# Kernel tuning notes

Hardware: AMD Instinct MI355X
Metric: run time of the kernel (lower is better)

The kernel has to match this reference:

```python
import jax, jax.numpy as jnp
import numpy as np

B, L, P, D, RD, NT = 128, 128, 1024, 128, 128, 256
SCALE = 1.0 / float(np.sqrt(D))


def _gelu(x):
    return jax.nn.gelu(x, approximate=False)


def _ln(x, g, b):
    mu = jnp.mean(x, axis=-1, keepdims=True)
    v = jnp.mean((x - mu) ** 2, axis=-1, keepdims=True)
    return (x - mu) * jax.lax.rsqrt(v + 1e-5) * g + b


def _mlp2(x, w1, b1, w2, b2):
    return _gelu(x @ w1 + b1) @ w2 + b2


def _l2norm(x):
    return x / jnp.maximum(jnp.sqrt(jnp.sum(x * x, axis=-1, keepdims=True)), 1e-12)


def _params(key):
    ks = jax.random.split(key, 16)
    def lin(k, i, o):
        return jax.random.normal(k, (i, o), jnp.float32) * (1.0 / float(np.sqrt(i)))
    z = lambda *s: jnp.zeros(s, jnp.float32)
    o = lambda *s: jnp.ones(s, jnp.float32)
    p = {}
    p['lt_emb'] = jax.random.normal(ks[0], (NT, D), jnp.float32) * 0.02
    p['lx_w1'] = lin(ks[1], 8, D); p['lx_b1'] = z(D)
    p['lx_w2'] = lin(ks[2], D, D); p['lx_b2'] = z(D)
    p['l_ln_g'] = o(D); p['l_ln_b'] = z(D)
    p['pt_emb'] = jax.random.normal(ks[3], (NT, D), jnp.float32) * 0.02
    p['px_w1'] = lin(ks[4], 192, D); p['px_b1'] = z(D)
    p['px_w2'] = lin(ks[5], D, D); p['px_b2'] = z(D)
    p['ps_w1'] = lin(ks[6], 1, D); p['ps_b1'] = z(D)
    p['ps_w2'] = lin(ks[7], D, D); p['ps_b2'] = z(D)
    p['p_ln_g'] = o(D); p['p_ln_b'] = z(D)
    p['proj_l_w'] = lin(ks[8], D, D)
    p['proj_p_w'] = lin(ks[9], D, D)
    p['dustbin_vec'] = jax.random.normal(ks[10], (D,), jnp.float32) * 0.02
    p['sg_w1'] = lin(ks[11], D, D); p['sg_b1'] = z(D)
    p['sg_w2'] = lin(ks[12], D, 1); p['sg_b2'] = z(1)
    p['retr_l_w'] = lin(ks[13], D, RD)
    p['retr_p_w'] = lin(ks[14], D, RD)
    return p


def setup_inputs():
    key = jax.random.key(0)
    kd = jax.random.split(key, 10)
    inp = {
        'l_x': jax.random.normal(kd[0], (B, L, 8), jnp.float32),
        'l_typ': jax.random.randint(kd[1], (B, L), 0, NT),
        'p_x': jax.random.normal(kd[2], (B, P, 192), jnp.float32),
        'p_typ': jax.random.randint(kd[3], (B, P), 0, NT),
        'p_score': jax.random.normal(kd[4], (B, P), jnp.float32),
        'p_rad': jax.random.uniform(kd[5], (B, P), jnp.float32),
        'l_mask': jax.random.bernoulli(kd[6], 0.9, (B, L)).at[:, 0].set(True),
        'p_mask': jax.random.bernoulli(kd[7], 0.9, (B, P)).at[:, 0].set(True),
    }
    inp.update(_params(kd[8]))
    return inp


def reference(l_x, l_typ, p_x, p_typ, p_score, p_rad, l_mask, p_mask,
              lt_emb, lx_w1, lx_b1, lx_w2, lx_b2, l_ln_g, l_ln_b,
              pt_emb, px_w1, px_b1, px_w2, px_b2, ps_w1, ps_b1, ps_w2, ps_b2,
              p_ln_g, p_ln_b, proj_l_w, proj_p_w, dustbin_vec,
              sg_w1, sg_b1, sg_w2, sg_b2, retr_l_w, retr_p_w):
    # --- encode_batch ---
    hL = _ln(_mlp2(l_x, lx_w1, lx_b1, lx_w2, lx_b2)
             + lt_emb[jnp.clip(l_typ, 0, NT - 1)], l_ln_g, l_ln_b) @ proj_l_w
    hP = _ln(_mlp2(p_x, px_w1, px_b1, px_w2, px_b2)
             + pt_emb[jnp.clip(p_typ, 0, NT - 1)]
             + _mlp2(p_score[..., None], ps_w1, ps_b1, ps_w2, ps_b2), p_ln_g, p_ln_b) @ proj_p_w
    neg = jnp.finfo(jnp.float32).min
    # --- feature_logits_batch: masked bilinear similarity ---
    logits = jnp.einsum('bld,bpd->blp', hL, hP) * SCALE  # [B,L,P]
    logits = jnp.where(p_mask[:, None, :], logits, neg)
    logits = jnp.where(l_mask[:, :, None], logits, neg)
    # --- assignment_logW_batch with dustbin ---
    dust = (hL @ dustbin_vec) * SCALE  # [B,L]
    full = jnp.concatenate([logits, dust[:, :, None]], axis=-1)  # [B,L,P+1]
    full = jnp.where(l_mask[:, :, None], full, neg)
    logW = jax.nn.log_softmax(full, axis=-1)
    # --- invariant_feature_terms_batch ---
    W = jnp.exp(logW)
    lm = l_mask.astype(jnp.float32)
    pm = p_mask.astype(jnp.float32)
    denom = jnp.maximum(lm.sum(axis=1), 1.0)  # [B]
    Wm = jnp.concatenate([W[..., :-1] * pm[:, None, :], W[..., -1:]], axis=-1)
    sharp = (Wm.max(axis=-1) * lm).sum(axis=1) / denom
    ent = ((-(Wm * logW)).sum(axis=-1) * lm).sum(axis=1) / denom
    neg_ent = -ent
    # --- pooled_embeddings_batch ---
    l_g = (hL * lm[..., None]).sum(axis=1) / jnp.maximum(lm.sum(axis=1)[:, None], 1.0)
    p_g = (hP * pm[..., None]).sum(axis=1) / jnp.maximum(pm.sum(axis=1)[:, None], 1.0)
    l_z = _l2norm(l_g @ retr_l_w)
    p_z = _l2norm(p_g @ retr_p_w)
    # --- pocket_sigma_nodes_batch ---
    sig = jax.nn.softplus((_gelu(hP @ sg_w1 + sg_b1) @ sg_w2 + sg_b2)[..., 0]) + 1e-3 + jnp.maximum(p_rad, 0.0)
    return logW, sharp, neg_ent, l_z, p_z, sig
```

## Files before the change

kernel.cpp:

```cpp
#include <hip/hip_runtime.h>
#include <hip/hip_bf16.h>
#include <math.h>

#define B_ 128
#define L_ 128
#define P_ 1024
#define D_ 128
#define NT_ 256

#define NEGF (-__FLT_MAX__)
#define SCALE_ 0.08838834764831845f
#define CLAMPV 1e30f

#define OUT_SHARP  16793600
#define OUT_NEGENT 16793728
#define OUT_LZ     16793856
#define OUT_PZ     16810240
#define OUT_SIG    16826624

#define WS_HLB    0
#define WS_HPB    1048576
#define WS_DUST   9437184
#define WS_SHARPP 9453568
#define WS_ENTP   9454592
#define WS_FLAG   9455616
#define WS_WT     9455632
#define WS_PPART  9500696
#define WS_PCNT   10024984

using bh8  = __attribute__((ext_vector_type(8))) short;
using fx4  = __attribute__((ext_vector_type(4))) float;

__device__ __forceinline__ float gelu_(float x) {
    float c = x * x;
    float v = x * fmaf(c, 0.07135481584f, 1.5957691216f);
    return x * __builtin_amdgcn_rcpf(1.0f + __expf(-v));
}
__device__ __forceinline__ float bf2f(unsigned short u) {
    return __uint_as_float(((unsigned)u) << 16);
}
__device__ __forceinline__ float sanz(float x) {
    return fminf(fmaxf(x, -CLAMPV), CLAMPV);
}
template<int BF> __device__ __forceinline__ float ldf(const void* p, int i) {
    if constexpr (BF) return bf2f(((const unsigned short*)p)[i]);
    else return ((const float*)p)[i];
}
template<int BF> __device__ __forceinline__ void stf(void* p, size_t i, float x) {
    x = sanz(x);
    if constexpr (BF) ((__hip_bfloat16*)p)[i] = __float2bfloat16(x);
    else ((float*)p)[i] = x;
}
__device__ __forceinline__ float maskf(const void* m, int mm, int idx) {
    if (mm == 3) return ((const float*)m)[idx] != 0.f ? 1.f : 0.f;
    if (mm == 2) return ((const unsigned short*)m)[idx] ? 1.f : 0.f;
    if (mm == 1) return ((const unsigned char*)m)[idx] ? 1.f : 0.f;
    return ((const int*)m)[idx] ? 1.f : 0.f;
}
__device__ __forceinline__ int typf(const void* p, int tm, int idx) {
    int v;
    if (tm == 2) v = (int)bf2f(((const unsigned short*)p)[idx]);
    else if (tm == 1) v = (int)((const long long*)p)[idx];
    else v = ((const int*)p)[idx];
    return v < 0 ? 0 : (v > NT_ - 1 ? NT_ - 1 : v);
}

__global__ __launch_bounds__(64) void detect_k(const unsigned int* __restrict__ px,
                                               const unsigned int* __restrict__ pm,
                                               const unsigned int* __restrict__ pt,
                                               int* __restrict__ flags)
{
    const int t = threadIdx.x;
    int hit = 0;
    for (int i = t; i < 4096; i += 64) {
        unsigned e = (px[i] >> 7) & 0xFFu;
        hit += (e >= 110 && e <= 132) ? 1 : 0;
    }
    for (int s = 1; s < 64; s <<= 1) hit += __shfl_xor(hit, s);

    unsigned big = 0, lo3f = 0, hi3f = 0;
    for (int i = t; i < 1024; i += 64) {
        unsigned wv = pm[i];
        big  |= (wv > 1u) ? 1u : 0u;
        lo3f |= ((wv & 0xFFFFu) == 0x3F80u) ? 1u : 0u;
        hi3f |= ((wv >> 16) == 0x3F80u) ? 1u : 0u;
    }
    unsigned long long aBig = __ballot(big != 0), aLo = __ballot(lo3f != 0), aHi = __ballot(hi3f != 0);

    unsigned tbig = 0, oddnz = 0;
    for (int i = t; i < 512; i += 64) {
        unsigned we = pt[2 * i], wo = pt[2 * i + 1];
        tbig  |= (we > 0xFFFFu || wo > 0xFFFFu) ? 1u : 0u;
        oddnz |= (wo != 0u) ? 1u : 0u;
    }
    unsigned long long aTb = __ballot(tbig != 0), aOdd = __ballot(oddnz != 0);

    if (t == 0) {
        flags[1] = (hit > 2048) ? 1 : 0;
        flags[0] = aLo ? 2 : (aHi ? 3 : (aBig ? 1 : 0));
        flags[2] = aTb ? 2 : (!aOdd ? 1 : 0);
    }
}

template<int BF> __device__ __forceinline__ void wt_prep_body(
    const void* w1, const void* w2, const void* sw2,
    const void* proj, const void* gw1, __hip_bfloat16* wt)
{
    const int idx = blockIdx.x * 256 + threadIdx.x;
    const int stride = gridDim.x * 256;
    for (int i = idx; i < 128 * 192; i += stride) {
        int n = i / 192, k = i - n * 192;
        wt[n * 192 + k] = __float2bfloat16(ldf<BF>(w1, k * 128 + n));
    }
    __hip_bfloat16* w2c = wt + 24576;
    for (int i = idx; i < 128 * 256; i += stride) {
        int n = i >> 8, k = i & 255;
        float v = (k < 128) ? ldf<BF>(w2, k * 128 + n) : ldf<BF>(sw2, (k - 128) * 128 + n);
        w2c[n * 256 + k] = __float2bfloat16(v);
    }
    __hip_bfloat16* pjt = wt + 57344;
    for (int i = idx; i < 128 * 128; i += stride) {
        int n = i >> 7, k = i & 127;
        pjt[n * 128 + k] = __float2bfloat16(ldf<BF>(proj, k * 128 + n));
    }
    __hip_bfloat16* g1t = wt + 73728;
    for (int i = idx; i < 128 * 128; i += stride) {
        int n = i >> 7, k = i & 127;
        g1t[n * 128 + k] = __float2bfloat16(ldf<BF>(gw1, k * 128 + n));
    }
}

__global__ __launch_bounds__(256) void wt_prep_k(
    const void* w1, const void* w2, const void* sw2,
    const void* proj, const void* gw1, __hip_bfloat16* wt, const int* flags)
{
    if (flags[1]) wt_prep_body<1>(w1, w2, sw2, proj, gw1, wt);
    else          wt_prep_body<0>(w1, w2, sw2, proj, gw1, wt);
}

#define RL 8
template<int BF> __device__ __forceinline__ void enc_l_body(
    const void* l_x, const void* l_typ, int tm,
    const void* w1, const void* b1, const void* w2, const void* b2,
    const void* lng, const void* lnb, const void* emb, const void* proj,
    const void* dustv, __hip_bfloat16* hLb, float* dust)
{
    __shared__ __align__(16) float X[RL * 8];
    __shared__ __align__(16) float H[RL][D_];
    __shared__ __align__(16) float Y[RL][D_];
    __shared__ float mus[RL], rss[RL];
    const int o = threadIdx.x;
    const int base = blockIdx.x * RL;

    if (o < RL * 8) X[o] = ldf<BF>(l_x, base * 8 + o);
    __syncthreads();

    float acc[RL];
    const float b1o = ldf<BF>(b1, o);
#pragma unroll
    for (int r = 0; r < RL; r++) acc[r] = b1o;
#pragma unroll
    for (int i = 0; i < 8; i += 4) {
        float wa = ldf<BF>(w1, (i + 0) * D_ + o), wb = ldf<BF>(w1, (i + 1) * D_ + o);
        float wc = ldf<BF>(w1, (i + 2) * D_ + o), wd = ldf<BF>(w1, (i + 3) * D_ + o);
#pragma unroll
        for (int r = 0; r < RL; r++) {
            const float4 x4 = *(const float4*)&X[r * 8 + i];
            acc[r] = fmaf(x4.x, wa, fmaf(x4.y, wb, fmaf(x4.z, wc, fmaf(x4.w, wd, acc[r]))));
        }
    }
#pragma unroll
    for (int r = 0; r < RL; r++) H[r][o] = gelu_(acc[r]);
    __syncthreads();

#pragma unroll
    for (int r = 0; r < RL; r++) {
        int tt = typf(l_typ, tm, base + r);
        acc[r] = ldf<BF>(b2, o) + ldf<BF>(emb, tt * D_ + o);
    }
    for (int i = 0; i < D_; i += 4) {
        float wa = ldf<BF>(w2, (i + 0) * D_ + o), wb = ldf<BF>(w2, (i + 1) * D_ + o);
        float wc = ldf<BF>(w2, (i + 2) * D_ + o), wd = ldf<BF>(w2, (i + 3) * D_ + o);
#pragma unroll
        for (int r = 0; r < RL; r++) {
            const float4 h4 = *(const float4*)&H[r][i];
            acc[r] = fmaf(h4.x, wa, fmaf(h4.y, wb, fmaf(h4.z, wc, fmaf(h4.w, wd, acc[r]))));
        }
    }
#pragma unroll
    for (int r = 0; r < RL; r++) Y[r][o] = acc[r];
    __syncthreads();

    {
        const int r = o >> 4, j = o & 15;
        float s = 0.f;
#pragma unroll
        for (int i = 0; i < 8; i++) s += Y[r][j * 8 + i];
        s += __shfl_xor(s, 1); s += __shfl_xor(s, 2); s += __shfl_xor(s, 4); s += __shfl_xor(s, 8);
        const float mu = s * (1.f / 128.f);
        float v = 0.f;
#pragma unroll
        for (int i = 0; i < 8; i++) { float d = Y[r][j * 8 + i] - mu; v = fmaf(d, d, v); }
        v += __shfl_xor(v, 1); v += __shfl_xor(v, 2); v += __shfl_xor(v, 4); v += __shfl_xor(v, 8);
        if (j == 0) { mus[r] = mu; rss[r] = rsqrtf(v * (1.f / 128.f) + 1e-5f); }
    }
    __syncthreads();
    {
        const float g = ldf<BF>(lng, o), bl = ldf<BF>(lnb, o);
#pragma unroll
        for (int r = 0; r < RL; r++) Y[r][o] = fmaf((Y[r][o] - mus[r]) * rss[r], g, bl);
    }
    __syncthreads();

#pragma unroll
    for (int r = 0; r < RL; r++) acc[r] = 0.f;
    for (int i = 0; i < D_; i += 4) {
        float wa = ldf<BF>(proj, (i + 0) * D_ + o), wb = ldf<BF>(proj, (i + 1) * D_ + o);
        float wc = ldf<BF>(proj, (i + 2) * D_ + o), wd = ldf<BF>(proj, (i + 3) * D_ + o);
#pragma unroll
        for (int r = 0; r < RL; r++) {
            const float4 y4 = *(const float4*)&Y[r][i];
            acc[r] = fmaf(y4.x, wa, fmaf(y4.y, wb, fmaf(y4.z, wc, fmaf(y4.w, wd, acc[r]))));
        }
    }
    const float dvo = ldf<BF>(dustv, o);
#pragma unroll
    for (int r = 0; r < RL; r++) {
        hLb[(size_t)(base + r) * D_ + o] = __float2bfloat16(acc[r]);
        H[r][o] = acc[r] * dvo;
    }
    __syncthreads();
    {
        const int r = o >> 4, j = o & 15;
        float s = 0.f;
#pragma unroll
        for (int i = 0; i < 8; i++) s += H[r][j * 8 + i];
        s += __shfl_xor(s, 1); s += __shfl_xor(s, 2); s += __shfl_xor(s, 4); s += __shfl_xor(s, 8);
        if (j == 0) dust[base + r] = s * SCALE_;
    }
}

__global__ __launch_bounds__(128) void enc_l_k(
    const void* l_x, const void* l_typ,
    const void* w1, const void* b1, const void* w2, const void* b2,
    const void* lng, const void* lnb, const void* emb, const void* proj,
    const void* dustv, __hip_bfloat16* hLb, float* dust, const int* flags)
{
    const int tm = flags[2];
    if (flags[1]) enc_l_body<1>(l_x, l_typ, tm, w1, b1, w2, b2, lng, lnb, emb, proj, dustv, hLb, dust);
    else          enc_l_body<0>(l_x, l_typ, tm, w1, b1, w2, b2, lng, lnb, emb, proj, dustv, hLb, dust);
}

#define XS 264
#define ROWS 32
#define ENC_P_SMEM 18304
template<int BF> __device__ __forceinline__ void enc_p_body(
    unsigned short* X, float* red1, float* red2, float* pm_s, float* sc_s, int* tt_s,
    const void* p_x, const void* p_typ, int tm,
    const void* p_score, const void* p_rad,
    const void* b1, const void* b2, const void* sb2,
    const void* sw1, const void* sb1,
    const void* lng, const void* lnb, const void* emb,
    const void* gb1, const void* gw2, const void* gb2,
    const unsigned short* wt, const void* p_mask, int mm,
    void* out, __hip_bfloat16* hPb, float* ppart, float* pcnt)
{
    const int t = threadIdx.x;
    const int o = t & 127, rh = t >> 7;
    const int lane = t & 63, w = t >> 6;
    const int m = lane & 15, g = lane >> 4;
    const int b = blockIdx.x >> 5, tile = blockIdx.x & 31;
    const int base = b * P_ + tile * ROWS;
    const int c0 = 32 * w + m, c1 = 32 * w + 16 + m;
    __hip_bfloat16* Xb = (__hip_bfloat16*)X;

    for (int i = t; i < ROWS * 192; i += 256) {
        int r = i / 192, k = i - r * 192;
        Xb[r * XS + k] = __float2bfloat16(ldf<BF>(p_x, (base + r) * 192 + k));
    }
    if (t < ROWS) {
        pm_s[t] = maskf(p_mask, mm, base + t);
        sc_s[t] = ldf<BF>(p_score, base + t);
        tt_s[t] = typf(p_typ, tm, base + t);
    }
    __syncthreads();

    fx4 A1[2][2];
#pragma unroll
    for (int mt = 0; mt < 2; mt++) { A1[mt][0] = fx4{0,0,0,0}; A1[mt][1] = fx4{0,0,0,0}; }
    {
        const unsigned short* w1T = wt;
        bh8 bf[12];
#pragma unroll
        for (int ks = 0; ks < 6; ks++) {
            bf[ks * 2 + 0] = *(const bh8*)(w1T + ((2 * w + 0) * 16 + m) * 192 + g * 8 + ks * 32);
            bf[ks * 2 + 1] = *(const bh8*)(w1T + ((2 * w + 1) * 16 + m) * 192 + g * 8 + ks * 32);
        }
#pragma unroll
        for (int mt = 0; mt < 2; mt++) {
            const unsigned short* xr = X + (mt * 16 + m) * XS + g * 8;
#pragma unroll
            for (int ks = 0; ks < 6; ks++) {
                bh8 a = *(const bh8*)(xr + ks * 32);
                A1[mt][0] = __builtin_amdgcn_mfma_f32_16x16x32_bf16(a, bf[ks * 2 + 0], A1[mt][0], 0, 0, 0);
                A1[mt][1] = __builtin_amdgcn_mfma_f32_16x16x32_bf16(a, bf[ks * 2 + 1], A1[mt][1], 0, 0, 0);
            }
        }
    }
    __syncthreads();

    {
        const float bb0 = ldf<BF>(b1, c0), bb1 = ldf<BF>(b1, c1);
#pragma unroll
        for (int mt = 0; mt < 2; mt++)
#pragma unroll
            for (int j = 0; j < 4; j++) {
                const int row = mt * 16 + g * 4 + j;
                Xb[row * XS + c0] = __float2bfloat16(gelu_(A1[mt][0][j] + bb0));
                Xb[row * XS + c1] = __float2bfloat16(gelu_(A1[mt][1][j] + bb1));
            }
    }
    {
        const float a1v = ldf<BF>(sw1, o), a0v = ldf<BF>(sb1, o);
#pragma unroll
        for (int r = 0; r < 16; r++) {
            const int row = rh * 16 + r;
            Xb[row * XS + 128 + o] = __float2bfloat16(gelu_(fmaf(sc_s[row], a1v, a0v)));
        }
    }
    __syncthreads();

    fx4 A2[2][2];
#pragma unroll
    for (int mt = 0; mt < 2; mt++) { A2[mt][0] = fx4{0,0,0,0}; A2[mt][1] = fx4{0,0,0,0}; }
    {
        const unsigned short* w2cT = wt + 24576;
        bh8 bf[16];
#pragma unroll
        for (int ks = 0; ks < 8; ks++) {
            bf[ks * 2 + 0] = *(const bh8*)(w2cT + ((2 * w + 0) * 16 + m) * 256 + g * 8 + ks * 32);
            bf[ks * 2 + 1] = *(const bh8*)(w2cT + ((2 * w + 1) * 16 + m) * 256 + g * 8 + ks * 32);
        }
#pragma unroll
        for (int mt = 0; mt < 2; mt++) {
            const unsigned short* xr = X + (mt * 16 + m) * XS + g * 8;
#pragma unroll
            for (int ks = 0; ks < 8; ks++) {
                bh8 a = *(const bh8*)(xr + ks * 32);
                A2[mt][0] = __builtin_amdgcn_mfma_f32_16x16x32_bf16(a, bf[ks * 2 + 0], A2[mt][0], 0, 0, 0);
                A2[mt][1] = __builtin_amdgcn_mfma_f32_16x16x32_bf16(a, bf[ks * 2 + 1], A2[mt][1], 0, 0, 0);
            }
        }
    }
    {
        const float bc0 = ldf<BF>(b2, c0) + ldf<BF>(sb2, c0);
        const float bc1 = ldf<BF>(b2, c1) + ldf<BF>(sb2, c1);
#pragma unroll
        for (int mt = 0; mt < 2; mt++)
#pragma unroll
            for (int j = 0; j < 4; j++) {
                const int row = mt * 16 + g * 4 + j;
                const int tt = tt_s[row];
                A2[mt][0][j] += bc0 + ldf<BF>(emb, tt * D_ + c0);
                A2[mt][1][j] += bc1 + ldf<BF>(emb, tt * D_ + c1);
            }
    }
#pragma unroll
    for (int mt = 0; mt < 2; mt++)
#pragma unroll
        for (int j = 0; j < 4; j++) {
            float s = A2[mt][0][j] + A2[mt][1][j];
            s += __shfl_xor(s, 1); s += __shfl_xor(s, 2); s += __shfl_xor(s, 4); s += __shfl_xor(s, 8);
            if (m == 0) red1[(mt * 16 + g * 4 + j) * 4 + w] = s;
        }
    __syncthreads();
    float mu_[2][4];
#pragma unroll
    for (int mt = 0; mt < 2; mt++)
#pragma unroll
        for (int j = 0; j < 4; j++) {
            const int row = mt * 16 + g * 4 + j;
            mu_[mt][j] = ((red1[row * 4 + 0] + red1[row * 4 + 1]) +
                          (red1[row * 4 + 2] + red1[row * 4 + 3])) * (1.f / 128.f);
            float d0 = A2[mt][0][j] - mu_[mt][j];
            float d1 = A2[mt][1][j] - mu_[mt][j];
            float v = fmaf(d0, d0, d1 * d1);
            v += __shfl_xor(v, 1); v += __shfl_xor(v, 2); v += __shfl_xor(v, 4); v += __shfl_xor(v, 8);
            if (m == 0) red2[row * 4 + w] = v;
        }
    __syncthreads();
    {
        const float gc0 = ldf<BF>(lng, c0), bl0 = ldf<BF>(lnb, c0);
        const float gc1 = ldf<BF>(lng, c1), bl1 = ldf<BF>(lnb, c1);
#pragma unroll
        for (int mt = 0; mt < 2; mt++)
#pragma unroll
            for (int j = 0; j < 4; j++) {
                const int row = mt * 16 + g * 4 + j;
                float var = ((red2[row * 4 + 0] + red2[row * 4 + 1]) +
                             (red2[row * 4 + 2] + red2[row * 4 + 3])) * (1.f / 128.f);
                float rs = rsqrtf(var + 1e-5f);
                float y0 = fmaf((A2[mt][0][j] - mu_[mt][j]) * rs, gc0, bl0);
                float y1 = fmaf((A2[mt][1][j] - mu_[mt][j]) * rs, gc1, bl1);
                Xb[row * XS + c0] = __float2bfloat16(y0);
                Xb[row * XS + c1] = __float2bfloat16(y1);
            }
    }
    __syncthreads();

    fx4 A3[2][2];
#pragma unroll
    for (int mt = 0; mt < 2; mt++) { A3[mt][0] = fx4{0,0,0,0}; A3[mt][1] = fx4{0,0,0,0}; }
    {
        const unsigned short* pjT = wt + 57344;
        bh8 bf[8];
#pragma unroll
        for (int ks = 0; ks < 4; ks++) {
            bf[ks * 2 + 0] = *(const bh8*)(pjT + ((2 * w + 0) * 16 + m) * 128 + g * 8 + ks * 32);
            bf[ks * 2 + 1] = *(const bh8*)(pjT + ((2 * w + 1) * 16 + m) * 128 + g * 8 + ks * 32);
        }
#pragma unroll
        for (int mt = 0; mt < 2; mt++) {
            const unsigned short* xr = X + (mt * 16 + m) * XS + g * 8;
#pragma unroll
            for (int ks = 0; ks < 4; ks++) {
                bh8 a = *(const bh8*)(xr + ks * 32);
                A3[mt][0] = __builtin_amdgcn_mfma_f32_16x16x32_bf16(a, bf[ks * 2 + 0], A3[mt][0], 0, 0, 0);
                A3[mt][1] = __builtin_amdgcn_mfma_f32_16x16x32_bf16(a, bf[ks * 2 + 1], A3[mt][1], 0, 0, 0);
            }
        }
    }
    __syncthreads();

    {
#pragma unroll
        for (int mt = 0; mt < 2; mt++)
#pragma unroll
            for (int j = 0; j < 4; j++) {
                const int row = mt * 16 + g * 4 + j;
                __hip_bfloat16 h0 = __float2bfloat16(A3[mt][0][j]);
                __hip_bfloat16 h1 = __float2bfloat16(A3[mt][1][j]);
                hPb[(size_t)(base + row) * D_ + c0] = h0;
                hPb[(size_t)(base + row) * D_ + c1] = h1;
                Xb[row * XS + c0] = h0;
                Xb[row * XS + c1] = h1;
            }
        float ps0 = 0.f, ps1 = 0.f;
#pragma unroll
        for (int mt = 0; mt < 2; mt++)
#pragma unroll
            for (int j = 0; j < 4; j++) {
                const int row = mt * 16 + g * 4 + j;
                ps0 = fmaf(A3[mt][0][j], pm_s[row], ps0);
                ps1 = fmaf(A3[mt][1][j], pm_s[row], ps1);
            }
        ps0 += __shfl_xor(ps0, 16); ps0 += __shfl_xor(ps0, 32);
        ps1 += __shfl_xor(ps1, 16); ps1 += __shfl_xor(ps1, 32);
        if (g == 0) {
            ppart[(size_t)blockIdx.x * D_ + c0] = ps0;
            ppart[(size_t)blockIdx.x * D_ + c1] = ps1;
        }
        if (t == 0) {
            float c = 0.f;
#pragma unroll
            for (int r = 0; r < ROWS; r++) c += pm_s[r];
            pcnt[blockIdx.x] = c;
        }
    }
    __syncthreads();

    fx4 A4[2][2];
#pragma unroll
    for (int mt = 0; mt < 2; mt++) { A4[mt][0] = fx4{0,0,0,0}; A4[mt][1] = fx4{0,0,0,0}; }
    {
        const unsigned short* g1T = wt + 73728;
        bh8 bf[8];
#pragma unroll
        for (int ks = 0; ks < 4; ks++) {
            bf[ks * 2 + 0] = *(const bh8*)(g1T + ((2 * w + 0) * 16 + m) * 128 + g * 8 + ks * 32);
            bf[ks * 2 + 1] = *(const bh8*)(g1T + ((2 * w + 1) * 16 + m) * 128 + g * 8 + ks * 32);
        }
#pragma unroll
        for (int mt = 0; mt < 2; mt++) {
            const unsigned short* xr = X + (mt * 16 + m) * XS + g * 8;
#pragma unroll
            for (int ks = 0; ks < 4; ks++) {
                bh8 a = *(const bh8*)(xr + ks * 32);
                A4[mt][0] = __builtin_amdgcn_mfma_f32_16x16x32_bf16(a, bf[ks * 2 + 0], A4[mt][0], 0, 0, 0);
                A4[mt][1] = __builtin_amdgcn_mfma_f32_16x16x32_bf16(a, bf[ks * 2 + 1], A4[mt][1], 0, 0, 0);
            }
        }
    }
    {
        const float gb0 = ldf<BF>(gb1, c0), gb1v = ldf<BF>(gb1, c1);
        const float w20 = ldf<BF>(gw2, c0), w21 = ldf<BF>(gw2, c1);
#pragma unroll
        for (int mt = 0; mt < 2; mt++)
#pragma unroll
            for (int j = 0; j < 4; j++) {
                const int row = mt * 16 + g * 4 + j;
                float g0 = gelu_(A4[mt][0][j] + gb0);
                float g1v = gelu_(A4[mt][1][j] + gb1v);
                float p = fmaf(g0, w20, g1v * w21);
                p += __shfl_xor(p, 1); p += __shfl_xor(p, 2); p += __shfl_xor(p, 4); p += __shfl_xor(p, 8);
                if (m == 0) red1[row * 4 + w] = p;
            }
    }
    __syncthreads();
    if (t < ROWS) {
        float s = (red1[t * 4 + 0] + red1[t * 4 + 1]) + (red1[t * 4 + 2] + red1[t * 4 + 3]);
        float v = s + ldf<BF>(gb2, 0);
        float sp = fmaxf(v, 0.f) + log1pf(expf(-fabsf(v)));
        stf<BF>(out, (size_t)OUT_SIG + base + t, sp + 1e-3f + fmaxf(ldf<BF>(p_rad, base + t), 0.f));
    }
}

__global__ __launch_bounds__(256) void enc_p_k(
    const void* p_x, const void* p_typ, const void* p_score, const void* p_rad,
    const void* b1, const void* b2, const void* sb2,
    const void* sw1, const void* sb1,
    const void* lng, const void* lnb, const void* emb,
    const void* gb1, const void* gw2, const void* gb2,
    const unsigned short* wt, const void* p_mask, const int* flags,
    void* out, __hip_bfloat16* hPb, float* ppart, float* pcnt)
{
    extern __shared__ __align__(16) char smem[];
    unsigned short* X = (unsigned short*)smem;
    float* red1 = (float*)(smem + 16896);
    float* red2 = (float*)(smem + 17408);
    float* pm_s = (float*)(smem + 17920);
    float* sc_s = (float*)(smem + 18048);
    int*   tt_s = (int*)(smem + 18176);
    const int tm = flags[2], mm = flags[0];
    if (flags[1]) enc_p_body<1>(X, red1, red2, pm_s, sc_s, tt_s,
                                p_x, p_typ, tm, p_score, p_rad, b1, b2, sb2, sw1, sb1,
                                lng, lnb, emb, gb1, gw2, gb2, wt, p_mask, mm,
                                out, hPb, ppart, pcnt);
    else          enc_p_body<0>(X, red1, red2, pm_s, sc_s, tt_s,
                                p_x, p_typ, tm, p_score, p_rad, b1, b2, sb2, sw1, sb1,
                                lng, lnb, emb, gb1, gw2, gb2, wt, p_mask, mm,
                                out, hPb, ppart, pcnt);
}

template<int BF> __device__ __forceinline__ void logits_sm_body(
    const unsigned short* hLb, const unsigned short* hPb, const float* dust,
    const void* l_mask, const void* p_mask, int mm,
    void* out, float* sharp_parts, float* ent_parts)
{
    __shared__ float pm_s[1024];
    __shared__ float lm_s[16], dv_s[16];
    __shared__ float redA[64], redB[64], redC[64], redD[64], redM[16], redL[16];
    const int t = threadIdx.x;
    const int lane = t & 63, w = t >> 6;
    const int m = lane & 15, g = lane >> 4;
    const int b = blockIdx.x & 127, l0 = (blockIdx.x >> 7) * 16;

    for (int i = t; i < 1024; i += 256) pm_s[i] = maskf(p_mask, mm, b * P_ + i);
    if (t < 16) {
        lm_s[t] = maskf(l_mask, mm, b * L_ + l0 + t);
        dv_s[t] = dust[b * L_ + l0 + t];
    }
    __syncthreads();

    bh8 af[4];
    {
        const unsigned short* ha = hLb + ((size_t)(b * L_ + l0 + m)) * D_ + g * 8;
#pragma unroll
        for (int ks = 0; ks < 4; ks++) af[ks] = *(const bh8*)(ha + ks * 32);
    }
    const unsigned short* hpb = hPb + ((size_t)(b * P_ + w * 256)) * D_;

    fx4 acc[16];
#pragma unroll
    for (int nt = 0; nt < 16; nt++) {
        fx4 c = {0.f, 0.f, 0.f, 0.f};
        const unsigned short* hr = hpb + (nt * 16 + m) * D_ + g * 8;
#pragma unroll
        for (int ks = 0; ks < 4; ks++) {
            bh8 bfr = *(const bh8*)(hr + ks * 32);
            c = __builtin_amdgcn_mfma_f32_16x16x32_bf16(af[ks], bfr, c, 0, 0, 0);
        }
        acc[nt] = c;
    }

    float rmax[4] = {NEGF, NEGF, NEGF, NEGF};
#pragma unroll
    for (int nt = 0; nt < 16; nt++) {
        const float pv = pm_s[w * 256 + nt * 16 + m];
#pragma unroll
        for (int j = 0; j < 4; j++) {
            const bool ok = (lm_s[g * 4 + j] != 0.f) && (pv != 0.f);
            float v = ok ? acc[nt][j] * SCALE_ : NEGF;
            acc[nt][j] = v;
            rmax[j] = fmaxf(rmax[j], v);
        }
    }
#pragma unroll
    for (int j = 0; j < 4; j++) {
        rmax[j] = fmaxf(rmax[j], __shfl_xor(rmax[j], 1));
        rmax[j] = fmaxf(rmax[j], __shfl_xor(rmax[j], 2));
        rmax[j] = fmaxf(rmax[j], __shfl_xor(rmax[j], 4));
        rmax[j] = fmaxf(rmax[j], __shfl_xor(rmax[j], 8));
    }
    if (m == 0) {
#pragma unroll
        for (int j = 0; j < 4; j++) redA[(g * 4 + j) * 4 + w] = rmax[j];
    }
    __syncthreads();
    float mrow[4], lse[4];
#pragma unroll
    for (int j = 0; j < 4; j++) {
        const int r = g * 4 + j;
        float mm4 = fmaxf(fmaxf(redA[r * 4 + 0], redA[r * 4 + 1]), fmaxf(redA[r * 4 + 2], redA[r * 4 + 3]));
        float dvr = (lm_s[r] != 0.f) ? dv_s[r] : NEGF;
        mrow[j] = fmaxf(mm4, dvr);
    }
    float se[4] = {0.f, 0.f, 0.f, 0.f};
#pragma unroll
    for (int nt = 0; nt < 16; nt++) {
#pragma unroll
        for (int j = 0; j < 4; j++) se[j] += __expf(acc[nt][j] - mrow[j]);
    }
#pragma unroll
    for (int j = 0; j < 4; j++) {
        se[j] += __shfl_xor(se[j], 1); se[j] += __shfl_xor(se[j], 2);
        se[j] += __shfl_xor(se[j], 4); se[j] += __shfl_xor(se[j], 8);
    }
    if (m == 0) {
#pragma unroll
        for (int j = 0; j < 4; j++) redB[(g * 4 + j) * 4 + w] = se[j];
    }
    __syncthreads();
#pragma unroll
    for (int j = 0; j < 4; j++) {
        const int r = g * 4 + j;
        float dvr = (lm_s[r] != 0.f) ? dv_s[r] : NEGF;
        float s = (redB[r * 4 + 0] + redB[r * 4 + 1]) + (redB[r * 4 + 2] + redB[r * 4 + 3]);
        s += __expf(dvr - mrow[j]);
        lse[j] = __logf(s);
    }
    if (w == 0 && m == 0) {
#pragma unroll
        for (int j = 0; j < 4; j++) { redM[g * 4 + j] = mrow[j]; redL[g * 4 + j] = lse[j]; }
    }
    float mw[4] = {0.f, 0.f, 0.f, 0.f}, es[4] = {0.f, 0.f, 0.f, 0.f};
#pragma unroll
    for (int nt = 0; nt < 16; nt++) {
        const float pv = pm_s[w * 256 + nt * 16 + m];
#pragma unroll
        for (int j = 0; j < 4; j++) {
            float lw = acc[nt][j] - mrow[j] - lse[j];
            stf<BF>(out, (size_t)(b * L_ + l0 + g * 4 + j) * (P_ + 1) + w * 256 + nt * 16 + m, lw);
            float lwc = fmaxf(lw, -CLAMPV);
            float wm = __expf(lwc) * pv;
            mw[j] = fmaxf(mw[j], wm);
            if (wm > 0.f) es[j] = fmaf(-wm, lwc, es[j]);
        }
    }
#pragma unroll
    for (int j = 0; j < 4; j++) {
        mw[j] = fmaxf(mw[j], __shfl_xor(mw[j], 1));
        mw[j] = fmaxf(mw[j], __shfl_xor(mw[j], 2));
        mw[j] = fmaxf(mw[j], __shfl_xor(mw[j], 4));
        mw[j] = fmaxf(mw[j], __shfl_xor(mw[j], 8));
        es[j] += __shfl_xor(es[j], 1); es[j] += __shfl_xor(es[j], 2);
        es[j] += __shfl_xor(es[j], 4); es[j] += __shfl_xor(es[j], 8);
    }
    if (m == 0) {
#pragma unroll
        for (int j = 0; j < 4; j++) {
            redC[(g * 4 + j) * 4 + w] = mw[j];
            redD[(g * 4 + j) * 4 + w] = es[j];
        }
    }
    __syncthreads();
    if (t < 16) {
        float dvr = (lm_s[t] != 0.f) ? dv_s[t] : NEGF;
        stf<BF>(out, (size_t)(b * L_ + l0 + t) * (P_ + 1) + P_, dvr - redM[t] - redL[t]);
    }
    if (t == 0) {
        float sp = 0.f, en = 0.f;
        for (int r = 0; r < 16; r++) {
            float dvr = (lm_s[r] != 0.f) ? dv_s[r] : NEGF;
            float lwd = fmaxf(dvr - redM[r] - redL[r], -CLAMPV);
            float wd = __expf(lwd);
            float mwr = fmaxf(fmaxf(redC[r * 4 + 0], redC[r * 4 + 1]), fmaxf(redC[r * 4 + 2], redC[r * 4 + 3]));
            mwr = fmaxf(mwr, wd);
            float esr = (redD[r * 4 + 0] + redD[r * 4 + 1]) + (redD[r * 4 + 2] + redD[r * 4 + 3]);
            if (wd > 0.f) esr = fmaf(-wd, lwd, esr);
            sp = fmaf(mwr, lm_s[r], sp);
            en = fmaf(esr, lm_s[r], en);
        }
        sharp_parts[blockIdx.x] = sp;
        ent_parts[blockIdx.x] = en;
    }
}

__global__ __launch_bounds__(256) void logits_sm_k(
    const unsigned short* hLb, const unsigned short* hPb, const float* dust,
    const void* l_mask, const void* p_mask, const int* flags,
    void* out, float* sharp_parts, float* ent_parts)
{
    const int mm = flags[0];
    if (flags[1]) logits_sm_body<1>(hLb, hPb, dust, l_mask, p_mask, mm, out, sharp_parts, ent_parts);
    else          logits_sm_body<0>(hLb, hPb, dust, l_mask, p_mask, mm, out, sharp_parts, ent_parts);
}

template<int BF> __device__ __forceinline__ void epilogue_body(
    const unsigned short* hLb, const void* l_mask, int mm,
    const void* retr_l, const void* retr_p,
    const float* ppart, const float* pcnt,
    const float* sharp_parts, const float* ent_parts, void* out)
{
    __shared__ float lmv[L_];
    __shared__ __align__(16) float lg[D_];
    __shared__ __align__(16) float pgs[D_];
    __shared__ float red[4];
    const int o = threadIdx.x, b = blockIdx.x;
    lmv[o] = maskf(l_mask, mm, b * L_ + o);
    __syncthreads();
    float cnt = 0.f;
    for (int l = 0; l < L_; l++) cnt += lmv[l];
    {
        float s0 = 0, s1 = 0, s2 = 0, s3 = 0;
        const unsigned short* hb = hLb + (size_t)b * L_ * D_;
        for (int l = 0; l < L_; l += 4) {
            s0 = fmaf(bf2f(hb[(l + 0) * D_ + o]), lmv[l + 0], s0);
            s1 = fmaf(bf2f(hb[(l + 1) * D_ + o]), lmv[l + 1], s1);
            s2 = fmaf(bf2f(hb[(l + 2) * D_ + o]), lmv[l + 2], s2);
            s3 = fmaf(bf2f(hb[(l + 3) * D_ + o]), lmv[l + 3], s3);
        }
        lg[o] = ((s0 + s1) + (s2 + s3)) / fmaxf(cnt, 1.f);
    }
    {
        float s = 0.f, c = 0.f;
        for (int k = 0; k < 32; k++) s += ppart[(size_t)(b * 32 + k) * D_ + o];
        for (int k = 0; k < 32; k++) c += pcnt[b * 32 + k];
        pgs[o] = s / fmaxf(c, 1.f);
    }
    __syncthreads();
    float rL = 0.f, rP = 0.f;
    for (int i = 0; i < D_; i += 4) {
        const float4 g4 = *(const float4*)&lg[i];
        rL = fmaf(g4.x, ldf<BF>(retr_l, (i + 0) * D_ + o), rL);
        rL = fmaf(g4.y, ldf<BF>(retr_l, (i + 1) * D_ + o), rL);
        rL = fmaf(g4.z, ldf<BF>(retr_l, (i + 2) * D_ + o), rL);
        rL = fmaf(g4.w, ldf<BF>(retr_l, (i + 3) * D_ + o), rL);
        const float4 p4 = *(const float4*)&pgs[i];
        rP = fmaf(p4.x, ldf<BF>(retr_p, (i + 0) * D_ + o), rP);
        rP = fmaf(p4.y, ldf<BF>(retr_p, (i + 1) * D_ + o), rP);
        rP = fmaf(p4.z, ldf<BF>(retr_p, (i + 2) * D_ + o), rP);
        rP = fmaf(p4.w, ldf<BF>(retr_p, (i + 3) * D_ + o), rP);
    }
    float nL = rL * rL, nP = rP * rP;
    nL += __shfl_xor(nL, 1); nL += __shfl_xor(nL, 2); nL += __shfl_xor(nL, 4);
    nL += __shfl_xor(nL, 8); nL += __shfl_xor(nL, 16); nL += __shfl_xor(nL, 32);
    nP += __shfl_xor(nP, 1); nP += __shfl_xor(nP, 2); nP += __shfl_xor(nP, 4);
    nP += __shfl_xor(nP, 8); nP += __shfl_xor(nP, 16); nP += __shfl_xor(nP, 32);
    if ((o & 63) == 0) { red[o >> 6] = nL; red[2 + (o >> 6)] = nP; }
    __syncthreads();
    {
        float nrmL = fmaxf(sqrtf(red[0] + red[1]), 1e-12f);
        float nrmP = fmaxf(sqrtf(red[2] + red[3]), 1e-12f);
        stf<BF>(out, (size_t)OUT_LZ + b * D_ + o, rL / nrmL);
        stf<BF>(out, (size_t)OUT_PZ + b * D_ + o, rP / nrmP);
    }
    if (o == 0) {
        const float den = fmaxf(cnt, 1.f);
        float sp = 0.f, en = 0.f;
        for (int k = 0; k < 8; k++) { sp += sharp_parts[k * 128 + b]; en += ent_parts[k * 128 + b]; }
        stf<BF>(out, (size_t)OUT_SHARP + b, sp / den);
        stf<BF>(out, (size_t)OUT_NEGENT + b, -(en / den));
    }
}

__global__ __launch_bounds__(128) void epilogue_k(
    const unsigned short* hLb, const void* l_mask, const int* flags,
    const void* retr_l, const void* retr_p,
    const float* ppart, const float* pcnt,
    const float* sharp_parts, const float* ent_parts, void* out)
{
    const int mm = flags[0];
    if (flags[1]) epilogue_body<1>(hLb, l_mask, mm, retr_l, retr_p, ppart, pcnt, sharp_parts, ent_parts, out);
    else          epilogue_body<0>(hLb, l_mask, mm, retr_l, retr_p, ppart, pcnt, sharp_parts, ent_parts, out);
}

extern "C" void kernel_launch(void* const* d_in, const int* in_sizes, int n_in,
                              void* d_out, int out_size, void* d_ws, size_t ws_size,
                              hipStream_t stream)
{
    const void* l_x     = d_in[0];
    const void* l_typ   = d_in[1];
    const void* p_x     = d_in[2];
    const void* p_typ   = d_in[3];
    const void* p_score = d_in[4];
    const void* p_rad   = d_in[5];
    const void* l_mask  = d_in[6];
    const void* p_mask  = d_in[7];
    const void* lt_emb  = d_in[8];
    const void* lx_w1   = d_in[9];
    const void* lx_b1   = d_in[10];
    const void* lx_w2   = d_in[11];
    const void* lx_b2   = d_in[12];
    const void* l_ln_g  = d_in[13];
    const void* l_ln_b  = d_in[14];
    const void* pt_emb  = d_in[15];
    const void* px_w1   = d_in[16];
    const void* px_b1   = d_in[17];
    const void* px_w2   = d_in[18];
    const void* px_b2   = d_in[19];
    const void* ps_w1   = d_in[20];
    const void* ps_b1   = d_in[21];
    const void* ps_w2   = d_in[22];
    const void* ps_b2   = d_in[23];
    const void* p_ln_g  = d_in[24];
    const void* p_ln_b  = d_in[25];
    const void* proj_l  = d_in[26];
    const void* proj_p  = d_in[27];
    const void* dustv   = d_in[28];
    const void* sg_w1   = d_in[29];
    const void* sg_b1   = d_in[30];
    const void* sg_w2   = d_in[31];
    const void* sg_b2   = d_in[32];
    const void* retr_l  = d_in[33];
    const void* retr_p  = d_in[34];

    float* ws     = (float*)d_ws;
    __hip_bfloat16* hLb = (__hip_bfloat16*)(ws + WS_HLB);
    __hip_bfloat16* hPb = (__hip_bfloat16*)(ws + WS_HPB);
    float* dust   = ws + WS_DUST;
    float* sharpp = ws + WS_SHARPP;
    float* entp   = ws + WS_ENTP;
    int*   flags  = (int*)(ws + WS_FLAG);
    __hip_bfloat16* wt = (__hip_bfloat16*)(ws + WS_WT);
    float* ppart  = ws + WS_PPART;
    float* pcnt   = ws + WS_PCNT;

    detect_k<<<1, 64, 0, stream>>>((const unsigned int*)p_x, (const unsigned int*)p_mask,
                                   (const unsigned int*)p_typ, flags);
    wt_prep_k<<<64, 256, 0, stream>>>(px_w1, px_w2, ps_w2, proj_p, sg_w1, wt, flags);
    enc_l_k<<<(B_ * L_) / RL, 128, 0, stream>>>(l_x, l_typ, lx_w1, lx_b1, lx_w2, lx_b2,
                                                l_ln_g, l_ln_b, lt_emb, proj_l, dustv,
                                                hLb, dust, flags);
    enc_p_k<<<B_ * (P_ / ROWS), 256, ENC_P_SMEM, stream>>>(
        p_x, p_typ, p_score, p_rad,
        px_b1, px_b2, ps_b2, ps_w1, ps_b1,
        p_ln_g, p_ln_b, pt_emb,
        sg_b1, sg_w2, sg_b2,
        (const unsigned short*)wt, p_mask, flags,
        d_out, hPb, ppart, pcnt);
    logits_sm_k<<<B_ * 8, 256, 0, stream>>>((const unsigned short*)hLb, (const unsigned short*)hPb,
                                            dust, l_mask, p_mask, flags, d_out, sharpp, entp);
    epilogue_k<<<B_, 128, 0, stream>>>((const unsigned short*)hLb, l_mask, flags,
                                       retr_l, retr_p, ppart, pcnt, sharpp, entp, d_out);
}
```

Before: 220.5 us.

## Double pocket encoder row tile to 64 and vectorize bf16 input staging

Each pocket-encoder block now handles 64 rows instead of 32, halving the grid. Each weight fragment loaded from global is reused across four MFMA row tiles instead of two, and the weights are streamed per k-step rather than preloaded in full. The bf16 input path copies eight elements per vector load into shared memory, and the pooled-partials reduction is updated to 16 tiles per batch. In exchange, shared memory doubles, accumulator register pressure rises, and fewer blocks are available to fill the GPU.

```diff
diff --git a/kernel.cpp b/kernel.cpp
--- a/kernel.cpp
+++ b/kernel.cpp
@@ -252,8 +252,8 @@
 }
 
 #define XS 264
-#define ROWS 32
-#define ENC_P_SMEM 18304
+#define ROWS 64
+#define ENC_P_SMEM 36608
 template<int BF> __device__ __forceinline__ void enc_p_body(
     unsigned short* X, float* red1, float* red2, float* pm_s, float* sc_s, int* tt_s,
     const void* p_x, const void* p_typ, int tm,
@@ -269,14 +269,23 @@
     const int o = t & 127, rh = t >> 7;
     const int lane = t & 63, w = t >> 6;
     const int m = lane & 15, g = lane >> 4;
-    const int b = blockIdx.x >> 5, tile = blockIdx.x & 31;
+    const int b = blockIdx.x >> 4, tile = blockIdx.x & 15;
     const int base = b * P_ + tile * ROWS;
     const int c0 = 32 * w + m, c1 = 32 * w + 16 + m;
     __hip_bfloat16* Xb = (__hip_bfloat16*)X;
 
-    for (int i = t; i < ROWS * 192; i += 256) {
-        int r = i / 192, k = i - r * 192;
-        Xb[r * XS + k] = __float2bfloat16(ldf<BF>(p_x, (base + r) * 192 + k));
+    if constexpr (BF) {
+        const unsigned short* src = (const unsigned short*)p_x + (size_t)base * 192;
+#pragma unroll
+        for (int i = t * 8; i < ROWS * 192; i += 256 * 8) {
+            const int r = i / 192, k = i - r * 192;
+            *(bh8*)(X + r * XS + k) = *(const bh8*)(src + i);
+        }
+    } else {
+        for (int i = t; i < ROWS * 192; i += 256) {
+            int r = i / 192, k = i - r * 192;
+            Xb[r * XS + k] = __float2bfloat16(((const float*)p_x)[(size_t)base * 192 + i]);
+        }
     }
     if (t < ROWS) {
         pm_s[t] = maskf(p_mask, mm, base + t);
@@ -285,25 +294,21 @@
     }
     __syncthreads();
 
-    fx4 A1[2][2];
-#pragma unroll
-    for (int mt = 0; mt < 2; mt++) { A1[mt][0] = fx4{0,0,0,0}; A1[mt][1] = fx4{0,0,0,0}; }
-    {
-        const unsigned short* w1T = wt;
-        bh8 bf[12];
+    fx4 A1[4][2];
+#pragma unroll
+    for (int mt = 0; mt < 4; mt++) { A1[mt][0] = fx4{0,0,0,0}; A1[mt][1] = fx4{0,0,0,0}; }
+    {
+        const unsigned short* q0 = wt + ((2 * w + 0) * 16 + m) * 192 + g * 8;
+        const unsigned short* q1 = wt + ((2 * w + 1) * 16 + m) * 192 + g * 8;
 #pragma unroll
         for (int ks = 0; ks < 6; ks++) {
-            bf[ks * 2 + 0] = *(const bh8*)(w1T + ((2 * w + 0) * 16 + m) * 192 + g * 8 + ks * 32);
-            bf[ks * 2 + 1] = *(const bh8*)(w1T + ((2 * w + 1) * 16 + m) * 192 + g * 8 + ks * 32);
-        }
-#pragma unroll
-        for (int mt = 0; mt < 2; mt++) {
-            const unsigned short* xr = X + (mt * 16 + m) * XS + g * 8;
-#pragma unroll
-            for (int ks = 0; ks < 6; ks++) {
-                bh8 a = *(const bh8*)(xr + ks * 32);
-                A1[mt][0] = __builtin_amdgcn_mfma_f32_16x16x32_bf16(a, bf[ks * 2 + 0], A1[mt][0], 0, 0, 0);
-                A1[mt][1] = __builtin_amdgcn_mfma_f32_16x16x32_bf16(a, bf[ks * 2 + 1], A1[mt][1], 0, 0, 0);
+            bh8 f0 = *(const bh8*)(q0 + ks * 32);
+            bh8 f1 = *(const bh8*)(q1 + ks * 32);
+#pragma unroll
+            for (int mt = 0; mt < 4; mt++) {
+                bh8 a = *(const bh8*)(X + (mt * 16 + m) * XS + g * 8 + ks * 32);
+                A1[mt][0] = __builtin_amdgcn_mfma_f32_16x16x32_bf16(a, f0, A1[mt][0], 0, 0, 0);
+                A1[mt][1] = __builtin_amdgcn_mfma_f32_16x16x32_bf16(a, f1, A1[mt][1], 0, 0, 0);
             }
         }
     }
@@ -312,7 +317,7 @@
     {
         const float bb0 = ldf<BF>(b1, c0), bb1 = ldf<BF>(b1, c1);
 #pragma unroll
-        for (int mt = 0; mt < 2; mt++)
+        for (int mt = 0; mt < 4; mt++)
 #pragma unroll
             for (int j = 0; j < 4; j++) {
                 const int row = mt * 16 + g * 4 + j;
@@ -323,32 +328,29 @@
     {
         const float a1v = ldf<BF>(sw1, o), a0v = ldf<BF>(sb1, o);
 #pragma unroll
-        for (int r = 0; r < 16; r++) {
-            const int row = rh * 16 + r;
+        for (int r = 0; r < 32; r++) {
+            const int row = rh * 32 + r;
             Xb[row * XS + 128 + o] = __float2bfloat16(gelu_(fmaf(sc_s[row], a1v, a0v)));
         }
     }
     __syncthreads();
 
-    fx4 A2[2][2];
-#pragma unroll
-    for (int mt = 0; mt < 2; mt++) { A2[mt][0] = fx4{0,0,0,0}; A2[mt][1] = fx4{0,0,0,0}; }
+    fx4 A2[4][2];
+#pragma unroll
+    for (int mt = 0; mt < 4; mt++) { A2[mt][0] = fx4{0,0,0,0}; A2[mt][1] = fx4{0,0,0,0}; }
     {
         const unsigned short* w2cT = wt + 24576;
-        bh8 bf[16];
+        const unsigned short* q0 = w2cT + ((2 * w + 0) * 16 + m) * 256 + g * 8;
+        const unsigned short* q1 = w2cT + ((2 * w + 1) * 16 + m) * 256 + g * 8;
 #pragma unroll
         for (int ks = 0; ks < 8; ks++) {
-            bf[ks * 2 + 0] = *(const bh8*)(w2cT + ((2 * w + 0) * 16 + m) * 256 + g * 8 + ks * 32);
-            bf[ks * 2 + 1] = *(const bh8*)(w2cT + ((2 * w + 1) * 16 + m) * 256 + g * 8 + ks * 32);
-        }
-#pragma unroll
-        for (int mt = 0; mt < 2; mt++) {
-            const unsigned short* xr = X + (mt * 16 + m) * XS + g * 8;
-#pragma unroll
-            for (int ks = 0; ks < 8; ks++) {
-                bh8 a = *(const bh8*)(xr + ks * 32);
-                A2[mt][0] = __builtin_amdgcn_mfma_f32_16x16x32_bf16(a, bf[ks * 2 + 0], A2[mt][0], 0, 0, 0);
-                A2[mt][1] = __builtin_amdgcn_mfma_f32_16x16x32_bf16(a, bf[ks * 2 + 1], A2[mt][1], 0, 0, 0);
+            bh8 f0 = *(const bh8*)(q0 + ks * 32);
+            bh8 f1 = *(const bh8*)(q1 + ks * 32);
+#pragma unroll
+            for (int mt = 0; mt < 4; mt++) {
+                bh8 a = *(const bh8*)(X + (mt * 16 + m) * XS + g * 8 + ks * 32);
+                A2[mt][0] = __builtin_amdgcn_mfma_f32_16x16x32_bf16(a, f0, A2[mt][0], 0, 0, 0);
+                A2[mt][1] = __builtin_amdgcn_mfma_f32_16x16x32_bf16(a, f1, A2[mt][1], 0, 0, 0);
             }
         }
     }
@@ -356,7 +358,7 @@
         const float bc0 = ldf<BF>(b2, c0) + ldf<BF>(sb2, c0);
         const float bc1 = ldf<BF>(b2, c1) + ldf<BF>(sb2, c1);
 #pragma unroll
-        for (int mt = 0; mt < 2; mt++)
+        for (int mt = 0; mt < 4; mt++)
 #pragma unroll
             for (int j = 0; j < 4; j++) {
                 const int row = mt * 16 + g * 4 + j;
@@ -366,7 +368,7 @@
             }
     }
 #pragma unroll
-    for (int mt = 0; mt < 2; mt++)
+    for (int mt = 0; mt < 4; mt++)
 #pragma unroll
         for (int j = 0; j < 4; j++) {
             float s = A2[mt][0][j] + A2[mt][1][j];
@@ -374,9 +376,9 @@
             if (m == 0) red1[(mt * 16 + g * 4 + j) * 4 + w] = s;
         }
     __syncthreads();
-    float mu_[2][4];
-#pragma unroll
-    for (int mt = 0; mt < 2; mt++)
+    float mu_[4][4];
+#pragma unroll
+    for (int mt = 0; mt < 4; mt++)
 #pragma unroll
         for (int j = 0; j < 4; j++) {
             const int row = mt * 16 + g * 4 + j;
@@ -393,7 +395,7 @@
         const float gc0 = ldf<BF>(lng, c0), bl0 = ldf<BF>(lnb, c0);
         const float gc1 = ldf<BF>(lng, c1), bl1 = ldf<BF>(lnb, c1);
 #pragma unroll
-        for (int mt = 0; mt < 2; mt++)
+        for (int mt = 0; mt < 4; mt++)
 #pragma unroll
             for (int j = 0; j < 4; j++) {
                 const int row = mt * 16 + g * 4 + j;
@@ -408,33 +410,30 @@
     }
     __syncthreads();
 
-    fx4 A3[2][2];
-#pragma unroll
-    for (int mt = 0; mt < 2; mt++) { A3[mt][0] = fx4{0,0,0,0}; A3[mt][1] = fx4{0,0,0,0}; }
+    fx4 A3[4][2];
+#pragma unroll
+    for (int mt = 0; mt < 4; mt++) { A3[mt][0] = fx4{0,0,0,0}; A3[mt][1] = fx4{0,0,0,0}; }
     {
         const unsigned short* pjT = wt + 57344;
-        bh8 bf[8];
+        const unsigned short* q0 = pjT + ((2 * w + 0) * 16 + m) * 128 + g * 8;
+        const unsigned short* q1 = pjT + ((2 * w + 1) * 16 + m) * 128 + g * 8;
 #pragma unroll
         for (int ks = 0; ks < 4; ks++) {
-            bf[ks * 2 + 0] = *(const bh8*)(pjT + ((2 * w + 0) * 16 + m) * 128 + g * 8 + ks * 32);
-            bf[ks * 2 + 1] = *(const bh8*)(pjT + ((2 * w + 1) * 16 + m) * 128 + g * 8 + ks * 32);
-        }
-#pragma unroll
-        for (int mt = 0; mt < 2; mt++) {
-            const unsigned short* xr = X + (mt * 16 + m) * XS + g * 8;
-#pragma unroll
-            for (int ks = 0; ks < 4; ks++) {
-                bh8 a = *(const bh8*)(xr + ks * 32);
-                A3[mt][0] = __builtin_amdgcn_mfma_f32_16x16x32_bf16(a, bf[ks * 2 + 0], A3[mt][0], 0, 0, 0);
-                A3[mt][1] = __builtin_amdgcn_mfma_f32_16x16x32_bf16(a, bf[ks * 2 + 1], A3[mt][1], 0, 0, 0);
-            }
-        }
-    }
-    __syncthreads();
-
-    {
-#pragma unroll
-        for (int mt = 0; mt < 2; mt++)
+            bh8 f0 = *(const bh8*)(q0 + ks * 32);
+            bh8 f1 = *(const bh8*)(q1 + ks * 32);
+#pragma unroll
+            for (int mt = 0; mt < 4; mt++) {
+                bh8 a = *(const bh8*)(X + (mt * 16 + m) * XS + g * 8 + ks * 32);
+                A3[mt][0] = __builtin_amdgcn_mfma_f32_16x16x32_bf16(a, f0, A3[mt][0], 0, 0, 0);
+                A3[mt][1] = __builtin_amdgcn_mfma_f32_16x16x32_bf16(a, f1, A3[mt][1], 0, 0, 0);
+            }
+        }
+    }
+    __syncthreads();
+
+    {
+#pragma unroll
+        for (int mt = 0; mt < 4; mt++)
 #pragma unroll
             for (int j = 0; j < 4; j++) {
                 const int row = mt * 16 + g * 4 + j;
@@ -447,7 +446,7 @@
             }
         float ps0 = 0.f, ps1 = 0.f;
 #pragma unroll
-        for (int mt = 0; mt < 2; mt++)
+        for (int mt = 0; mt < 4; mt++)
 #pragma unroll
             for (int j = 0; j < 4; j++) {
                 const int row = mt * 16 + g * 4 + j;
@@ -469,25 +468,22 @@
     }
     __syncthreads();
 
-    fx4 A4[2][2];
-#pragma unroll
-    for (int mt = 0; mt < 2; mt++) { A4[mt][0] = fx4{0,0,0,0}; A4[mt][1] = fx4{0,0,0,0}; }
+    fx4 A4[4][2];
+#pragma unroll
+    for (int mt = 0; mt < 4; mt++) { A4[mt][0] = fx4{0,0,0,0}; A4[mt][1] = fx4{0,0,0,0}; }
     {
         const unsigned short* g1T = wt + 73728;
-        bh8 bf[8];
+        const unsigned short* q0 = g1T + ((2 * w + 0) * 16 + m) * 128 + g * 8;
+        const unsigned short* q1 = g1T + ((2 * w + 1) * 16 + m) * 128 + g * 8;
 #pragma unroll
         for (int ks = 0; ks < 4; ks++) {
-            bf[ks * 2 + 0] = *(const bh8*)(g1T + ((2 * w + 0) * 16 + m) * 128 + g * 8 + ks * 32);
-            bf[ks * 2 + 1] = *(const bh8*)(g1T + ((2 * w + 1) * 16 + m) * 128 + g * 8 + ks * 32);
-        }
-#pragma unroll
-        for (int mt = 0; mt < 2; mt++) {
-            const unsigned short* xr = X + (mt * 16 + m) * XS + g * 8;
-#pragma unroll
-            for (int ks = 0; ks < 4; ks++) {
-                bh8 a = *(const bh8*)(xr + ks * 32);
-                A4[mt][0] = __builtin_amdgcn_mfma_f32_16x16x32_bf16(a, bf[ks * 2 + 0], A4[mt][0], 0, 0, 0);
-                A4[mt][1] = __builtin_amdgcn_mfma_f32_16x16x32_bf16(a, bf[ks * 2 + 1], A4[mt][1], 0, 0, 0);
+            bh8 f0 = *(const bh8*)(q0 + ks * 32);
+            bh8 f1 = *(const bh8*)(q1 + ks * 32);
+#pragma unroll
+            for (int mt = 0; mt < 4; mt++) {
+                bh8 a = *(const bh8*)(X + (mt * 16 + m) * XS + g * 8 + ks * 32);
+                A4[mt][0] = __builtin_amdgcn_mfma_f32_16x16x32_bf16(a, f0, A4[mt][0], 0, 0, 0);
+                A4[mt][1] = __builtin_amdgcn_mfma_f32_16x16x32_bf16(a, f1, A4[mt][1], 0, 0, 0);
             }
         }
     }
@@ -495,7 +491,7 @@
         const float gb0 = ldf<BF>(gb1, c0), gb1v = ldf<BF>(gb1, c1);
         const float w20 = ldf<BF>(gw2, c0), w21 = ldf<BF>(gw2, c1);
 #pragma unroll
-        for (int mt = 0; mt < 2; mt++)
+        for (int mt = 0; mt < 4; mt++)
 #pragma unroll
             for (int j = 0; j < 4; j++) {
                 const int row = mt * 16 + g * 4 + j;
@@ -526,11 +522,11 @@
 {
     extern __shared__ __align__(16) char smem[];
     unsigned short* X = (unsigned short*)smem;
-    float* red1 = (float*)(smem + 16896);
-    float* red2 = (float*)(smem + 17408);
-    float* pm_s = (float*)(smem + 17920);
-    float* sc_s = (float*)(smem + 18048);
-    int*   tt_s = (int*)(smem + 18176);
+    float* red1 = (float*)(smem + 33792);
+    float* red2 = (float*)(smem + 34816);
+    float* pm_s = (float*)(smem + 35840);
+    float* sc_s = (float*)(smem + 36096);
+    int*   tt_s = (int*)(smem + 36352);
     const int tm = flags[2], mm = flags[0];
     if (flags[1]) enc_p_body<1>(X, red1, red2, pm_s, sc_s, tt_s,
                                 p_x, p_typ, tm, p_score, p_rad, b1, b2, sb2, sw1, sb1,
@@ -734,8 +730,8 @@
     }
     {
         float s = 0.f, c = 0.f;
-        for (int k = 0; k < 32; k++) s += ppart[(size_t)(b * 32 + k) * D_ + o];
-        for (int k = 0; k < 32; k++) c += pcnt[b * 32 + k];
+        for (int k = 0; k < 16; k++) s += ppart[(size_t)(b * 16 + k) * D_ + o];
+        for (int k = 0; k < 16; k++) c += pcnt[b * 16 + k];
         pgs[o] = s / fmaxf(c, 1.f);
     }
     __syncthreads();
```

Result: faster. 211.2 us (-4.2%).
